# Performance work log

Hardware: AMD Instinct MI355X
Metric: run time of the kernel (lower is better)

The kernel has to match this reference:

```python
import jax, jax.numpy as jnp
import numpy as np

B, IN_CAPS, IN_DIM = 64, 2048, 16
NUM_CAPS, OUT_DIM = 32, 16
NUM_ROUTING = 3


def squash(v, axis=-1):
    # scale = |v|^2 / (1 + |v|^2) / |v|  (faithful to source, no epsilon)
    s2 = jnp.sum(jnp.square(v), axis=axis, keepdims=True)
    scale = s2 / (1.0 + s2) / jnp.sqrt(s2)
    return scale * v


def setup_inputs() -> dict:
    key = jax.random.key(0)
    k1, k2 = jax.random.split(key)
    inputs = jax.random.normal(k1, (B, IN_CAPS, IN_DIM), dtype=jnp.float32)
    # glorot-ish scaled transform matrices
    W = jax.random.normal(k2, (IN_CAPS, NUM_CAPS, IN_DIM, OUT_DIM), dtype=jnp.float32) * 0.05
    return {"inputs": inputs, "W": W}


def reference(inputs, W):
    # Prediction vectors u_hat[b,i,k,:] = inputs[b,i,:] @ W[i,k,:,:]
    u_hat = jnp.einsum('bid,ikdo->biko', inputs, W)  # [B, I, K, O]
    # Routing logits b (per-batch; source initializes from zeros and accumulates agreement)
    b = jnp.zeros(u_hat.shape[:3], dtype=u_hat.dtype)  # [B, I, K]
    v = None
    for i in range(NUM_ROUTING):
        c = jax.nn.softmax(b, axis=2)                      # coupling coeffs over output caps K
        s = jnp.einsum('bik,biko->bko', c, u_hat)          # weighted sum over input caps I
        v = squash(s)                                      # [B, K, O]
        if i != NUM_ROUTING - 1:
            b = b + jnp.einsum('biko,bko->bik', u_hat, v)  # agreement update
    return v  # [B, NUM_CAPS, OUT_DIM]
```

## Files before the change

kernel.cpp:

```cpp
#include <hip/hip_runtime.h>
#include <math.h>
#include <stdint.h>

#define NB 64
#define NI 2048
#define NK 32
#define ND 16

typedef _Float16 h2t   __attribute__((ext_vector_type(2)));
typedef _Float16 f16x4 __attribute__((ext_vector_type(4)));
typedef float    f32x4 __attribute__((ext_vector_type(4)));

#if defined(__has_builtin)
#if __has_builtin(__builtin_amdgcn_global_load_lds)
#define HAVE_GLL 1
#endif
#endif
#ifndef HAVE_GLL
#define HAVE_GLL 0
#endif

static __device__ __forceinline__ uint32_t pack_h2(float a, float b) {
    h2t p; p.x = (_Float16)a; p.y = (_Float16)b;
    return __builtin_bit_cast(uint32_t, p);
}

static __device__ __forceinline__ float swz_xor16(float x) {
    int v = __builtin_amdgcn_ds_swizzle(__builtin_bit_cast(int, x), 0x401F);
    return __builtin_bit_cast(float, v);
}
static __device__ __forceinline__ float xreduce_o(float p) {
    p += swz_xor16(p);
    p += __shfl_xor(p, 32);
    return p;
}

__global__ __launch_bounds__(256)
void conv_w(const float* __restrict__ Wg, uint32_t* __restrict__ Wh)
{
    __shared__ float tile[32 * 264];
    const int i = blockIdx.x;
    const int t = threadIdx.x;
    const float4* src = (const float4*)(Wg + (size_t)i * 8192);
#pragma unroll
    for (int j = 0; j < 8; ++j) {
        const int f4 = t + j * 256;
        const int k  = f4 >> 6;
        const int r4 = f4 & 63;
        *(float4*)(&tile[k * 264 + r4 * 4]) = src[f4];
    }
    __syncthreads();
    const int T  = t >> 3;
    const int l0 = (t & 7) * 8;
    const float* s = tile + T * 264;
    uint2* dst = (uint2*)(Wh + (size_t)i * 4096) + T * 64 + l0;
#pragma unroll
    for (int n = 0; n < 8; ++n) {
        const int l = l0 + n;
        const int q = l >> 4, r = l & 15;
        uint2 u;
        u.x = pack_h2(s[(4 * q + 0) * 16 + r], s[(4 * q + 1) * 16 + r]);
        u.y = pack_h2(s[(4 * q + 2) * 16 + r], s[(4 * q + 3) * 16 + r]);
        dst[n] = u;
    }
}

__global__ __launch_bounds__(256)
void conv_x(const float* __restrict__ X, uint32_t* __restrict__ XT)
{
    const int g = blockIdx.x * 256 + threadIdx.x;
    const int b = g >> 11, i = g & 2047;
    const float4* src = (const float4*)(X + ((size_t)b * 2048 + i) * 16);
    const float4 f0 = src[0], f1 = src[1], f2 = src[2], f3 = src[3];
    uint4 o0, o1;
    o0.x = pack_h2(f0.x, f0.y); o0.y = pack_h2(f0.z, f0.w);
    o0.z = pack_h2(f1.x, f1.y); o0.w = pack_h2(f1.z, f1.w);
    o1.x = pack_h2(f2.x, f2.y); o1.y = pack_h2(f2.z, f2.w);
    o1.z = pack_h2(f3.x, f3.y); o1.w = pack_h2(f3.z, f3.w);
    uint4* dst = (uint4*)(XT + (size_t)i * 512 + b * 8);
    dst[0] = o0; dst[1] = o1;
}

template<int VMODE>
__global__ __launch_bounds__(256, 2)
void caps_pass_m(const uint32_t* __restrict__ XT,
                 const uint32_t* __restrict__ Wh,
                 const float* __restrict__ V,
                 uint32_t* __restrict__ part_h)
{
    constexpr int IC = 16;
    __shared__ uint32_t Ws[3][4096];
    __shared__ uint32_t Xs[2048];
    __shared__ float    Ep[2][4][16];

    const int t = threadIdx.x;
    const int l = t & 63;
    const int w = t >> 6;
    const int r = l & 15;
    const int q = l >> 4;

    const int wg     = blockIdx.x;
    const int xcd    = wg & 7;
    const int slot   = wg >> 3;
    const int ichunk = xcd * 16 + (slot >> 2);
    const int bg     = slot & 3;
    const int i0 = ichunk * IC;
    const int b0 = bg * 16;

    f32x4 s_acc[8];
#pragma unroll
    for (int tt = 0; tt < 8; ++tt) s_acc[tt] = (f32x4){0.f, 0.f, 0.f, 0.f};

    f32x4 v_r[8];
    if constexpr (VMODE == 1) {
#pragma unroll
        for (int tt = 0; tt < 8; ++tt)
            v_r[tt] = *(const f32x4*)(V + ((size_t)(b0 + r) * NK + (8 * w + tt)) * 16 + 4 * q);
    }

    {
        const int ig = t >> 4, uu = t & 15;
        const uint4* src = (const uint4*)(XT + (size_t)(i0 + ig) * 512 + b0 * 8);
        *(uint4*)&Xs[ig * 128 + uu * 4]        = src[uu];
        *(uint4*)&Xs[ig * 128 + (uu + 16) * 4] = src[uu + 16];
    }

#define STAGE_W(buf, tile)                                                     \
    {                                                                          \
        const size_t ibase_ = (size_t)(tile) * 4096;                           \
        _Pragma("unroll")                                                      \
        for (int j = 0; j < 4; ++j) {                                          \
            const int p = w * 4 + j;                                           \
            STAGE_ONE(buf, ibase_, p)                                          \
        }                                                                      \
    }
#if HAVE_GLL
#define STAGE_ONE(buf, ibase_, p)                                              \
    __builtin_amdgcn_global_load_lds(                                          \
        (const __attribute__((address_space(1))) void*)(Wh + ibase_ + (p) * 256 + l * 4), \
        (__attribute__((address_space(3))) void*)&Ws[buf][(p) * 256], 16, 0, 0);
#define BAR_W(n) asm volatile("s_waitcnt vmcnt(" #n ")\ns_barrier" ::: "memory");
#else
#define STAGE_ONE(buf, ibase_, p)                                              \
    ((uint4*)&Ws[buf][(p) * 256])[l] = *(const uint4*)(Wh + ibase_ + (p) * 256 + l * 4);
#define BAR_W(n) asm volatile("s_waitcnt vmcnt(0) lgkmcnt(0)\ns_barrier" ::: "memory");
#endif
#define BAR_E() asm volatile("s_waitcnt lgkmcnt(0)\ns_barrier" ::: "memory");

    __syncthreads();

    STAGE_W(0, i0)
    STAGE_W(1, i0 + 1)

    int cur = 0;
    for (int ii = 0; ii < IC; ++ii) {
        if (ii + 1 < IC) { BAR_W(4) } else { BAR_W(0) }

        if (ii + 2 < IC) {
            const int nslot = (cur + 2 >= 3) ? cur - 1 : cur + 2;
            STAGE_W(nslot, i0 + ii + 2)
        }

        const f16x4 xb = *(const f16x4*)&Xs[ii * 128 + r * 8 + q * 2];

        if constexpr (VMODE == 0) {
#pragma unroll
            for (int tt = 0; tt < 8; ++tt) {
                const f16x4 a = *(const f16x4*)&Ws[cur][(w * 8 + tt) * 128 + l * 2];
                s_acc[tt] = __builtin_amdgcn_mfma_f32_16x16x16f16(a, xb, s_acc[tt], 0, 0, 0);
            }
        } else {
            f32x4 um[8];
#pragma unroll
            for (int tt = 0; tt < 8; ++tt) {
                const f16x4 a = *(const f16x4*)&Ws[cur][(w * 8 + tt) * 128 + l * 2];
                um[tt] = __builtin_amdgcn_mfma_f32_16x16x16f16(
                    a, xb, (f32x4){0.f, 0.f, 0.f, 0.f}, 0, 0, 0);
            }
            float e[8];
            float esp = 0.f;
#pragma unroll
            for (int tt = 0; tt < 8; ++tt) {
                float p = um[tt][0] * v_r[tt][0];
                p = fmaf(um[tt][1], v_r[tt][1], p);
                p = fmaf(um[tt][2], v_r[tt][2], p);
                p = fmaf(um[tt][3], v_r[tt][3], p);
                p = xreduce_o(p);
                e[tt] = __expf(p);
                esp += e[tt];
            }
            if (q == 0) Ep[ii & 1][w][r] = esp;
            BAR_E();
            const float es = Ep[ii & 1][0][r] + Ep[ii & 1][1][r]
                           + Ep[ii & 1][2][r] + Ep[ii & 1][3][r];
            const float ci = __builtin_amdgcn_rcpf(es);
#pragma unroll
            for (int tt = 0; tt < 8; ++tt) {
                const float c = e[tt] * ci;
                s_acc[tt][0] = fmaf(c, um[tt][0], s_acc[tt][0]);
                s_acc[tt][1] = fmaf(c, um[tt][1], s_acc[tt][1]);
                s_acc[tt][2] = fmaf(c, um[tt][2], s_acc[tt][2]);
                s_acc[tt][3] = fmaf(c, um[tt][3], s_acc[tt][3]);
            }
        }
        cur = (cur == 2) ? 0 : cur + 1;
    }
#undef STAGE_W
#undef STAGE_ONE
#undef BAR_W
#undef BAR_E

    uint32_t* base = part_h + (size_t)(bg * 128 + ichunk) * 4096 + r * 256 + 2 * q;
#pragma unroll
    for (int tt = 0; tt < 8; ++tt) {
        uint2 st;
        st.x = pack_h2(s_acc[tt][0], s_acc[tt][1]);
        st.y = pack_h2(s_acc[tt][2], s_acc[tt][3]);
        *(uint2*)(base + (8 * w + tt) * 8) = st;
    }
}

template<int RMODE>
__global__ __launch_bounds__(256)
void caps_reduce(const uint32_t* __restrict__ part_h,
                 const float* __restrict__ S0red,
                 float* __restrict__ S0out,
                 float* __restrict__ Vout)
{
    __shared__ float2 red[4][64];
    const int t   = threadIdx.x;
    const int jl  = t & 63;
    const int qc  = t >> 6;
    const int jb  = blockIdx.x * 64;
    const int j   = jb + jl;
    const int b   = j >> 8;
    const int bg  = b >> 4;
    const int loc = (b & 15) * 256 + (j & 255);
    const uint32_t* p = part_h + ((size_t)(bg * 128 + qc * 32)) * 4096 + loc;
    float sx = 0.f, sy = 0.f;
#pragma unroll 8
    for (int ic = 0; ic < 32; ++ic) {
        h2t v = __builtin_bit_cast(h2t, p[(size_t)ic * 4096]);
        sx += (float)v.x; sy += (float)v.y;
    }
    red[qc][jl] = make_float2(sx, sy);
    __syncthreads();
    if (t < 64) {
        const int jj = jb + t;
        float2 a0 = red[0][t], a1 = red[1][t], a2 = red[2][t], a3 = red[3][t];
        const float tx = a0.x + a1.x + a2.x + a3.x;
        const float ty = a0.y + a1.y + a2.y + a3.y;
        if constexpr (RMODE == 0) {
            S0out[2 * jj]     = tx;
            S0out[2 * jj + 1] = ty;
            const float vx = tx * (1.0f / 32.0f), vy = ty * (1.0f / 32.0f);
            float sq = vx * vx + vy * vy;
#pragma unroll
            for (int mask = 4; mask >= 1; mask >>= 1) sq += __shfl_xor(sq, mask);
            const float sc = sqrtf(sq) / (1.0f + sq);
            Vout[2 * jj]     = vx * sc;
            Vout[2 * jj + 1] = vy * sc;
        } else if constexpr (RMODE == 1) {
            const float v0x = S0red[2 * jj] * (1.0f / 32.0f);
            const float v0y = S0red[2 * jj + 1] * (1.0f / 32.0f);
            float sq0 = v0x * v0x + v0y * v0y;
#pragma unroll
            for (int mask = 4; mask >= 1; mask >>= 1) sq0 += __shfl_xor(sq0, mask);
            const float sc0 = sqrtf(sq0) / (1.0f + sq0);
            float sq1 = tx * tx + ty * ty;
#pragma unroll
            for (int mask = 4; mask >= 1; mask >>= 1) sq1 += __shfl_xor(sq1, mask);
            const float sc1 = sqrtf(sq1) / (1.0f + sq1);
            Vout[2 * jj]     = fmaf(v0x, sc0, tx * sc1);
            Vout[2 * jj + 1] = fmaf(v0y, sc0, ty * sc1);
        } else {
            float sq = tx * tx + ty * ty;
#pragma unroll
            for (int mask = 4; mask >= 1; mask >>= 1) sq += __shfl_xor(sq, mask);
            const float sc = sqrtf(sq) / (1.0f + sq);
            Vout[2 * jj]     = tx * sc;
            Vout[2 * jj + 1] = ty * sc;
        }
    }
}

template<int VMODE>
__global__ __launch_bounds__(256, 4)
void caps_pass_f32(const float* __restrict__ X,
                   const float* __restrict__ Wg,
                   const float* __restrict__ S0,
                   const float* __restrict__ S1,
                   float* __restrict__ Sout)
{
    constexpr int IC = 8;
    __shared__ float Ws[8192];
    __shared__ float Xs[2048];

    const int t   = threadIdx.x;
    const int kk  = t & 31;
    const int oh  = (t >> 5) & 1;
    const int bq4 = t >> 6;

    const int wg     = blockIdx.x;
    const int xcd    = wg & 7;
    const int slot   = wg >> 3;
    const int ichunk = xcd * 32 + (slot >> 2);
    const int bg     = slot & 3;
    const int i0 = ichunk * IC;
    const int b0 = bg * 16;

    float s_acc[4][8];
#pragma unroll
    for (int bb = 0; bb < 4; ++bb)
#pragma unroll
        for (int o = 0; o < 8; ++o) s_acc[bb][o] = 0.f;

    float v_r[4][8];
    if constexpr (VMODE >= 1) {
#pragma unroll
        for (int bb = 0; bb < 4; ++bb) {
            const int b = b0 + bq4 * 4 + bb;
            const float* p0 = S0 + ((size_t)b * NK + kk) * 16 + oh * 8;
            float4 a = *(const float4*)(p0);
            float4 c = *(const float4*)(p0 + 4);
            float val0[8] = {a.x,a.y,a.z,a.w,c.x,c.y,c.z,c.w};
            float sq0 = 0.f;
#pragma unroll
            for (int o = 0; o < 8; ++o) { val0[o] *= (1.0f/32.0f); sq0 = fmaf(val0[o], val0[o], sq0); }
            sq0 += __shfl_xor(sq0, 32);
            const float sc0 = sqrtf(sq0) / (1.0f + sq0);
#pragma unroll
            for (int o = 0; o < 8; ++o) v_r[bb][o] = val0[o] * sc0;
            if constexpr (VMODE == 2) {
                const float* p1 = S1 + ((size_t)b * NK + kk) * 16 + oh * 8;
                float4 a1 = *(const float4*)(p1);
                float4 c1 = *(const float4*)(p1 + 4);
                float val1[8] = {a1.x,a1.y,a1.z,a1.w,c1.x,c1.y,c1.z,c1.w};
                float sq1 = 0.f;
#pragma unroll
                for (int o = 0; o < 8; ++o) sq1 = fmaf(val1[o], val1[o], sq1);
                sq1 += __shfl_xor(sq1, 32);
                const float sc1 = sqrtf(sq1) / (1.0f + sq1);
#pragma unroll
                for (int o = 0; o < 8; ++o) v_r[bb][o] = fmaf(val1[o], sc1, v_r[bb][o]);
            }
        }
    }

    {
        const int xb   = t >> 4;
        const int xig  = t & 7;
        const int half = (t >> 3) & 1;
        const float* xp = X + (size_t)(b0 + xb) * (NI * ND) + (size_t)(i0 + xig) * ND + half * 8;
        float4 f0 = *(const float4*)(xp);
        float4 f1 = *(const float4*)(xp + 4);
        float vals[8] = {f0.x,f0.y,f0.z,f0.w,f1.x,f1.y,f1.z,f1.w};
        const int m = (xig & 7) << 3;
#pragma unroll
        for (int jj = 0; jj < 8; ++jj) {
            const int d = half * 8 + jj;
            Xs[xig * 256 + ((16 * d + xb) ^ m)] = vals[jj];
        }
    }

    for (int ii = 0; ii < IC; ++ii) {
        const int i = i0 + ii;
        __syncthreads();
        {
            const float4* wsrc = (const float4*)(Wg + (size_t)i * 8192);
#pragma unroll
            for (int j = 0; j < 8; ++j) {
                float4 val = wsrc[t + j * 256];
                const int k = (t >> 6) + 4 * j;
                ((float4*)Ws)[k * 64 + ((t & 63) ^ (k & 7))] = val;
            }
        }
        __syncthreads();

        const int xm = (ii & 7) << 3;
        float u[4][8];
        if constexpr (VMODE >= 1) {
#pragma unroll
            for (int bb = 0; bb < 4; ++bb)
#pragma unroll
                for (int o = 0; o < 8; ++o) u[bb][o] = 0.f;
        }
#pragma unroll
        for (int d = 0; d < 16; ++d) {
            const float4 x4 = *(const float4*)(&Xs[ii * 256 + ((16 * d + 4 * bq4) ^ xm)]);
            float wvv[8];
            {
                const float4 wA = ((const float4*)Ws)[kk * 64 + ((d * 4 + oh * 2)     ^ (kk & 7))];
                const float4 wB = ((const float4*)Ws)[kk * 64 + ((d * 4 + oh * 2 + 1) ^ (kk & 7))];
                wvv[0]=wA.x; wvv[1]=wA.y; wvv[2]=wA.z; wvv[3]=wA.w;
                wvv[4]=wB.x; wvv[5]=wB.y; wvv[6]=wB.z; wvv[7]=wB.w;
            }
            if constexpr (VMODE >= 1) {
#pragma unroll
                for (int o = 0; o < 8; ++o) {
                    u[0][o] = fmaf(x4.x, wvv[o], u[0][o]);
                    u[1][o] = fmaf(x4.y, wvv[o], u[1][o]);
                    u[2][o] = fmaf(x4.z, wvv[o], u[2][o]);
                    u[3][o] = fmaf(x4.w, wvv[o], u[3][o]);
                }
            } else {
#pragma unroll
                for (int o = 0; o < 8; ++o) {
                    s_acc[0][o] = fmaf(x4.x, wvv[o], s_acc[0][o]);
                    s_acc[1][o] = fmaf(x4.y, wvv[o], s_acc[1][o]);
                    s_acc[2][o] = fmaf(x4.z, wvv[o], s_acc[2][o]);
                    s_acc[3][o] = fmaf(x4.w, wvv[o], s_acc[3][o]);
                }
            }
        }

        if constexpr (VMODE >= 1) {
#pragma unroll
            for (int bb = 0; bb < 4; ++bb) {
                float lg = 0.f;
#pragma unroll
                for (int o = 0; o < 8; ++o) lg = fmaf(u[bb][o], v_r[bb][o], lg);
                lg += __shfl_xor(lg, 32);
                float m = lg;
#pragma unroll
                for (int mask = 16; mask >= 1; mask >>= 1)
                    m = fmaxf(m, __shfl_xor(m, mask));
                const float e = __expf(lg - m);
                float ssum = e;
#pragma unroll
                for (int mask = 16; mask >= 1; mask >>= 1)
                    ssum += __shfl_xor(ssum, mask);
                const float c = e / ssum;
#pragma unroll
                for (int o = 0; o < 8; ++o)
                    s_acc[bb][o] = fmaf(c, u[bb][o], s_acc[bb][o]);
            }
        }
    }

#pragma unroll
    for (int bb = 0; bb < 4; ++bb) {
        float* sp = Sout + ((size_t)(b0 + bq4 * 4 + bb) * NK + kk) * 16 + oh * 8;
#pragma unroll
        for (int o = 0; o < 8; ++o) atomicAdd(sp + o, s_acc[bb][o]);
    }
}

__global__ __launch_bounds__(256)
void squash_kernel(const float* __restrict__ S, float* __restrict__ Vout)
{
    const int idx = blockIdx.x * 256 + threadIdx.x;
    float val = S[idx];
    float sq = val * val;
#pragma unroll
    for (int mask = 8; mask >= 1; mask >>= 1) sq += __shfl_xor(sq, mask);
    const float sc = sqrtf(sq) / (1.0f + sq);
    Vout[idx] = val * sc;
}

extern "C" void kernel_launch(void* const* d_in, const int* in_sizes, int n_in,
                              void* d_out, int out_size, void* d_ws, size_t ws_size,
                              hipStream_t stream)
{
    const float* X  = (const float*)d_in[0];
    const float* Wg = (const float*)d_in[1];
    float* out = (float*)d_out;

    const size_t WHU   = (size_t)2048 * 4096;
    const size_t XHU   = (size_t)64 * 2048 * 8;
    const size_t PARTU = (size_t)512 * 4096;
    const size_t need  = (WHU + XHU + PARTU) * 4 + 3 * 32768 * 4;

    const dim3 blk(256), pgrid(512), rgrid(256);

    if (ws_size >= need) {
        uint32_t* Wh   = (uint32_t*)d_ws;
        uint32_t* XT   = Wh + WHU;
        uint32_t* part = XT + XHU;
        float* s0      = (float*)(part + PARTU);
        float* v0      = s0 + 32768;
        float* v01     = v0 + 32768;

        conv_w<<<dim3(2048), blk, 0, stream>>>(Wg, Wh);
        conv_x<<<dim3(512),  blk, 0, stream>>>(X, XT);

        caps_pass_m<0><<<pgrid, blk, 0, stream>>>(XT, Wh, nullptr, part);
        caps_reduce<0><<<rgrid, blk, 0, stream>>>(part, nullptr, s0, v0);
        caps_pass_m<1><<<pgrid, blk, 0, stream>>>(XT, Wh, v0, part);
        caps_reduce<1><<<rgrid, blk, 0, stream>>>(part, s0, nullptr, v01);
        caps_pass_m<1><<<pgrid, blk, 0, stream>>>(XT, Wh, v01, part);
        caps_reduce<2><<<rgrid, blk, 0, stream>>>(part, nullptr, nullptr, out);
    } else {
        float* s0 = (float*)d_ws;
        float* s1 = s0 + 32768;
        float* s2 = s1 + 32768;
        hipMemsetAsync(d_ws, 0, (size_t)3 * 32768 * sizeof(float), stream);
        caps_pass_f32<0><<<dim3(1024), blk, 0, stream>>>(X, Wg, nullptr, nullptr, s0);
        caps_pass_f32<1><<<dim3(1024), blk, 0, stream>>>(X, Wg, s0, nullptr, s1);
        caps_pass_f32<2><<<dim3(1024), blk, 0, stream>>>(X, Wg, s0, s1, s2);
        squash_kernel<<<dim3(128), blk, 0, stream>>>(s2, out);
    }
}
```

Before: 96.75 us.

## Process input capsules in pairs with double-buffered W staging to halve barriers

Replaces the three-slot, one-tile-at-a-time W ring buffer with a two-slot buffer where each slot holds two consecutive input-capsule tiles. The loop is fully unrolled over pairs, so there is one W barrier and one softmax-sum barrier per pair instead of per tile. Softmax partial sums for both tiles are written to separate Ep slots before a single barrier. This is meant to cut synchronisation overhead and give the scheduler more independent MFMA work. In exchange it uses more LDS per block, keeps more values live in registers (um and e arrays doubled), and prefetches only one pair ahead.

```diff
diff --git a/kernel.cpp b/kernel.cpp
--- a/kernel.cpp
+++ b/kernel.cpp
@@ -89,7 +89,8 @@
                  uint32_t* __restrict__ part_h)
 {
     constexpr int IC = 16;
-    __shared__ uint32_t Ws[3][4096];
+    constexpr int NP = IC / 2;
+    __shared__ uint32_t Ws[2][2][4096];
     __shared__ uint32_t Xs[2048];
     __shared__ float    Ep[2][4][16];
 
@@ -125,88 +126,104 @@
         *(uint4*)&Xs[ig * 128 + (uu + 16) * 4] = src[uu + 16];
     }
 
-#define STAGE_W(buf, tile)                                                     \
+#if HAVE_GLL
+#define STAGE_T(sl, half, tile)                                                \
     {                                                                          \
         const size_t ibase_ = (size_t)(tile) * 4096;                           \
         _Pragma("unroll")                                                      \
         for (int j = 0; j < 4; ++j) {                                          \
             const int p = w * 4 + j;                                           \
-            STAGE_ONE(buf, ibase_, p)                                          \
+            __builtin_amdgcn_global_load_lds(                                  \
+                (const __attribute__((address_space(1))) void*)(Wh + ibase_ + p * 256 + l * 4), \
+                (__attribute__((address_space(3))) void*)&Ws[sl][half][p * 256], 16, 0, 0); \
         }                                                                      \
     }
-#if HAVE_GLL
-#define STAGE_ONE(buf, ibase_, p)                                              \
-    __builtin_amdgcn_global_load_lds(                                          \
-        (const __attribute__((address_space(1))) void*)(Wh + ibase_ + (p) * 256 + l * 4), \
-        (__attribute__((address_space(3))) void*)&Ws[buf][(p) * 256], 16, 0, 0);
 #define BAR_W(n) asm volatile("s_waitcnt vmcnt(" #n ")\ns_barrier" ::: "memory");
 #else
-#define STAGE_ONE(buf, ibase_, p)                                              \
-    ((uint4*)&Ws[buf][(p) * 256])[l] = *(const uint4*)(Wh + ibase_ + (p) * 256 + l * 4);
+#define STAGE_T(sl, half, tile)                                                \
+    {                                                                          \
+        const size_t ibase_ = (size_t)(tile) * 4096;                           \
+        _Pragma("unroll")                                                      \
+        for (int j = 0; j < 4; ++j) {                                          \
+            const int p = w * 4 + j;                                           \
+            ((uint4*)&Ws[sl][half][p * 256])[l] = *(const uint4*)(Wh + ibase_ + p * 256 + l * 4); \
+        }                                                                      \
+    }
 #define BAR_W(n) asm volatile("s_waitcnt vmcnt(0) lgkmcnt(0)\ns_barrier" ::: "memory");
 #endif
 #define BAR_E() asm volatile("s_waitcnt lgkmcnt(0)\ns_barrier" ::: "memory");
 
     __syncthreads();
 
-    STAGE_W(0, i0)
-    STAGE_W(1, i0 + 1)
-
-    int cur = 0;
-    for (int ii = 0; ii < IC; ++ii) {
-        if (ii + 1 < IC) { BAR_W(4) } else { BAR_W(0) }
-
-        if (ii + 2 < IC) {
-            const int nslot = (cur + 2 >= 3) ? cur - 1 : cur + 2;
-            STAGE_W(nslot, i0 + ii + 2)
-        }
-
-        const f16x4 xb = *(const f16x4*)&Xs[ii * 128 + r * 8 + q * 2];
+    STAGE_T(0, 0, i0 + 0) STAGE_T(0, 1, i0 + 1)
+    STAGE_T(1, 0, i0 + 2) STAGE_T(1, 1, i0 + 3)
+
+#pragma unroll
+    for (int j = 0; j < NP; ++j) {
+        const int s = j & 1;
+        if (j == 0) { BAR_W(8) } else { BAR_W(0) }
+
+        if (j >= 1 && j + 1 < NP) {
+            const int ns = (j + 1) & 1;
+            const int nt = i0 + 2 * (j + 1);
+            STAGE_T(ns, 0, nt) STAGE_T(ns, 1, nt + 1)
+        }
 
         if constexpr (VMODE == 0) {
 #pragma unroll
-            for (int tt = 0; tt < 8; ++tt) {
-                const f16x4 a = *(const f16x4*)&Ws[cur][(w * 8 + tt) * 128 + l * 2];
-                s_acc[tt] = __builtin_amdgcn_mfma_f32_16x16x16f16(a, xb, s_acc[tt], 0, 0, 0);
+            for (int ia = 0; ia < 2; ++ia) {
+                const int ii = 2 * j + ia;
+                const f16x4 xb = *(const f16x4*)&Xs[ii * 128 + r * 8 + q * 2];
+#pragma unroll
+                for (int tt = 0; tt < 8; ++tt) {
+                    const f16x4 a = *(const f16x4*)&Ws[s][ia][(w * 8 + tt) * 128 + l * 2];
+                    s_acc[tt] = __builtin_amdgcn_mfma_f32_16x16x16f16(a, xb, s_acc[tt], 0, 0, 0);
+                }
             }
         } else {
-            f32x4 um[8];
-#pragma unroll
-            for (int tt = 0; tt < 8; ++tt) {
-                const f16x4 a = *(const f16x4*)&Ws[cur][(w * 8 + tt) * 128 + l * 2];
-                um[tt] = __builtin_amdgcn_mfma_f32_16x16x16f16(
-                    a, xb, (f32x4){0.f, 0.f, 0.f, 0.f}, 0, 0, 0);
-            }
-            float e[8];
-            float esp = 0.f;
-#pragma unroll
-            for (int tt = 0; tt < 8; ++tt) {
-                float p = um[tt][0] * v_r[tt][0];
-                p = fmaf(um[tt][1], v_r[tt][1], p);
-                p = fmaf(um[tt][2], v_r[tt][2], p);
-                p = fmaf(um[tt][3], v_r[tt][3], p);
-                p = xreduce_o(p);
-                e[tt] = __expf(p);
-                esp += e[tt];
-            }
-            if (q == 0) Ep[ii & 1][w][r] = esp;
+            f32x4 um[2][8];
+            float e[2][8];
+#pragma unroll
+            for (int ia = 0; ia < 2; ++ia) {
+                const int ii = 2 * j + ia;
+                const f16x4 xb = *(const f16x4*)&Xs[ii * 128 + r * 8 + q * 2];
+#pragma unroll
+                for (int tt = 0; tt < 8; ++tt) {
+                    const f16x4 a = *(const f16x4*)&Ws[s][ia][(w * 8 + tt) * 128 + l * 2];
+                    um[ia][tt] = __builtin_amdgcn_mfma_f32_16x16x16f16(
+                        a, xb, (f32x4){0.f, 0.f, 0.f, 0.f}, 0, 0, 0);
+                }
+                float esp = 0.f;
+#pragma unroll
+                for (int tt = 0; tt < 8; ++tt) {
+                    float p = um[ia][tt][0] * v_r[tt][0];
+                    p = fmaf(um[ia][tt][1], v_r[tt][1], p);
+                    p = fmaf(um[ia][tt][2], v_r[tt][2], p);
+                    p = fmaf(um[ia][tt][3], v_r[tt][3], p);
+                    p = xreduce_o(p);
+                    e[ia][tt] = __expf(p);
+                    esp += e[ia][tt];
+                }
+                if (q == 0) Ep[ia][w][r] = esp;
+            }
             BAR_E();
-            const float es = Ep[ii & 1][0][r] + Ep[ii & 1][1][r]
-                           + Ep[ii & 1][2][r] + Ep[ii & 1][3][r];
-            const float ci = __builtin_amdgcn_rcpf(es);
-#pragma unroll
-            for (int tt = 0; tt < 8; ++tt) {
-                const float c = e[tt] * ci;
-                s_acc[tt][0] = fmaf(c, um[tt][0], s_acc[tt][0]);
-                s_acc[tt][1] = fmaf(c, um[tt][1], s_acc[tt][1]);
-                s_acc[tt][2] = fmaf(c, um[tt][2], s_acc[tt][2]);
-                s_acc[tt][3] = fmaf(c, um[tt][3], s_acc[tt][3]);
-            }
-        }
-        cur = (cur == 2) ? 0 : cur + 1;
-    }
-#undef STAGE_W
-#undef STAGE_ONE
+#pragma unroll
+            for (int ia = 0; ia < 2; ++ia) {
+                const float es = Ep[ia][0][r] + Ep[ia][1][r]
+                               + Ep[ia][2][r] + Ep[ia][3][r];
+                const float ci = __builtin_amdgcn_rcpf(es);
+#pragma unroll
+                for (int tt = 0; tt < 8; ++tt) {
+                    const float c = e[ia][tt] * ci;
+                    s_acc[tt][0] = fmaf(c, um[ia][tt][0], s_acc[tt][0]);
+                    s_acc[tt][1] = fmaf(c, um[ia][tt][1], s_acc[tt][1]);
+                    s_acc[tt][2] = fmaf(c, um[ia][tt][2], s_acc[tt][2]);
+                    s_acc[tt][3] = fmaf(c, um[ia][tt][3], s_acc[tt][3]);
+                }
+            }
+        }
+    }
+#undef STAGE_T
 #undef BAR_W
 #undef BAR_E
 
```

After: 341.0 us. +252.5%, slower.
